# Kernel tuning notes

Measured on AMD Instinct MI355X. Metric: run time of the kernel, lower is better.

## Reference

```python
import jax, jax.numpy as jnp
import numpy as np

N_NODES = 100000
N_EDGES = 3200000
D_FEAT = 128
N1 = 128
N2 = 64
NUM_CLASSES = 10
NUM_GRAPHS = 256


def gcn_conv(x, edge_index, W, b, num_nodes):
    """PyG GCNConv: y = D^-1/2 (A+I) D^-1/2 (x W) + b, self-loops added."""
    src, dst = edge_index[0], edge_index[1]
    # degree including self-loop (edge weight 1)
    deg = jax.ops.segment_sum(jnp.ones_like(dst, dtype=x.dtype), dst,
                              num_segments=num_nodes) + 1.0
    dis = jnp.where(deg > 0, deg ** -0.5, 0.0)  # deg_inv_sqrt, [N]
    h = x @ W                                    # transform first, [N, out]
    norm = dis[src] * dis[dst]                   # [E]
    msg = h[src] * norm[:, None]                 # gather + scale, [E, out]
    agg = jax.ops.segment_sum(msg, dst, num_segments=num_nodes)
    agg = agg + h * (dis * dis)[:, None]         # self-loop contribution
    return agg + b


def global_mean_pool(x, batch, num_graphs):
    sums = jax.ops.segment_sum(x, batch, num_segments=num_graphs)
    cnt = jax.ops.segment_sum(jnp.ones((x.shape[0],), dtype=x.dtype), batch,
                              num_segments=num_graphs)
    return sums / jnp.maximum(cnt, 1.0)[:, None]


def setup_inputs() -> dict:
    key = jax.random.key(0)
    ks = jax.random.split(key, 8)
    x = jax.random.normal(ks[0], (N_NODES, D_FEAT), dtype=jnp.float32)
    edge_index = jax.random.randint(ks[1], (2, N_EDGES), 0, N_NODES, dtype=jnp.int64)
    batch = jnp.sort(jax.random.randint(ks[2], (N_NODES,), 0, NUM_GRAPHS, dtype=jnp.int64))
    W1 = jax.random.normal(ks[3], (D_FEAT, N1), dtype=jnp.float32) / np.sqrt(D_FEAT)
    b1 = jnp.zeros((N1,), dtype=jnp.float32)
    W2 = jax.random.normal(ks[4], (N1, N2), dtype=jnp.float32) / np.sqrt(N1)
    b2 = jnp.zeros((N2,), dtype=jnp.float32)
    Wfc = jax.random.normal(ks[5], (N2, NUM_CLASSES), dtype=jnp.float32) / np.sqrt(N2)
    bfc = jnp.zeros((NUM_CLASSES,), dtype=jnp.float32)
    return {"x": x, "edge_index": edge_index, "batch": batch,
            "W1": W1, "b1": b1, "W2": W2, "b2": b2,
            "Wfc": Wfc, "bfc": bfc, "num_graphs": NUM_GRAPHS}


def reference(x, edge_index, batch, W1, b1, W2, b2, Wfc, bfc, num_graphs):
    n = x.shape[0]
    h = gcn_conv(x, edge_index, W1, b1, n)
    h = jax.nn.relu(h)
    h = gcn_conv(h, edge_index, W2, b2, n)
    g = global_mean_pool(h, batch, num_graphs)   # [num_graphs, N2]
    # dropout is identity at inference
    return g @ Wfc + bfc                          # [num_graphs, num_classes]
```

## Files before the change

kernel.cpp:

```cpp
#include <hip/hip_runtime.h>
#include <math.h>

typedef unsigned int  u32;
typedef unsigned short u16;

#define TILE1 8192
#define BKW   256
#define CAP   9216

typedef __attribute__((ext_vector_type(8))) short bf16x8;
typedef __attribute__((ext_vector_type(4))) float f32x4;
typedef __attribute__((ext_vector_type(2))) float f32x2;
union frag_u { bf16x8 v; u32 u[4]; uint4 q; };

__device__ inline u32 bf16_rne(float f) {
    u32 u = __float_as_uint(f);
    return (u + 0x7FFFu + ((u >> 16) & 1u)) >> 16;
}
__device__ inline float bf_lo(u32 u) { return __uint_as_float(u << 16); }
__device__ inline float bf_hi(u32 u) { return __uint_as_float(u & 0xFFFF0000u); }

__device__ inline f32x2 up2(u32 u) {
    f32x2 t;
    t.x = __uint_as_float(u << 16);
    t.y = __uint_as_float(u & 0xFFFF0000u);
    return t;
}
__device__ inline void add8p(f32x2* a, uint4 q) {
    a[0] += up2(q.x); a[1] += up2(q.y); a[2] += up2(q.z); a[3] += up2(q.w);
}

__device__ inline u32 relu_pk(u32 v) {
    u32 s = v & 0x80008000u;
    u32 m = (s >> 15) * 0xFFFFu;
    return v & ~m;
}


__global__ __launch_bounds__(512) void k_part1(const int* __restrict__ ei,
                                               int* __restrict__ bucketCur,
                                               u32* __restrict__ tmp,
                                               int E, int N, int NBK) {
    __shared__ int hist[1024];
    __shared__ int base[512];
    const int tid = threadIdx.x;
    if (tid < NBK) { hist[tid] = 0; hist[512 + tid] = 0; }
    __syncthreads();

    const int rep = (tid & 1) << 9;
    const int t0 = blockIdx.x * TILE1;
    const int4* ei4s = (const int4*)ei;
    const int4* ei4d = (const int4*)(ei + E);
    const int q0 = t0 >> 2;
    const int QE = E >> 2;

    int sv[16], dv[16], key[16];
#pragma unroll
    for (int j = 0; j < 4; ++j) {
        int qi = q0 + j * 512 + tid;
        int4 s4 = make_int4(0, 0, 0, 0), d4 = make_int4(-1, -1, -1, -1);
        if (qi < QE) { s4 = ei4s[qi]; d4 = ei4d[qi]; }
        sv[4 * j + 0] = s4.x; dv[4 * j + 0] = d4.x;
        sv[4 * j + 1] = s4.y; dv[4 * j + 1] = d4.y;
        sv[4 * j + 2] = s4.z; dv[4 * j + 2] = d4.z;
        sv[4 * j + 3] = s4.w; dv[4 * j + 3] = d4.w;
    }
#pragma unroll
    for (int j = 0; j < 16; ++j) {
        key[j] = -1;
        if ((unsigned)dv[j] < (unsigned)N && (unsigned)sv[j] < (unsigned)N) {
            key[j] = dv[j] >> 8;
            atomicAdd(&hist[key[j] + rep], 1);
        }
    }
    __syncthreads();
    if (tid < NBK) {
        int tot = hist[tid] + hist[512 + tid];
        base[tid] = atomicAdd(&bucketCur[tid], tot);
        hist[tid] = 0;
    }
    __syncthreads();
#pragma unroll
    for (int j = 0; j < 16; ++j) {
        if (key[j] >= 0) {
            int slot = atomicAdd(&hist[key[j]], 1);
            int off = base[key[j]] + slot;
            if (off < CAP)
                tmp[(size_t)key[j] * CAP + off] =
                    ((u32)(dv[j] & 255) << 17) | (u32)sv[j];
        }
    }
}

__global__ __launch_bounds__(512) void k_part2(const int* __restrict__ bucketCnt,
                                               const u32* __restrict__ tmp,
                                               int* __restrict__ csr,
                                               int* __restrict__ rowptr,
                                               float* __restrict__ dis,
                                               int N, int NBK) {
    __shared__ int hist[256];
    __shared__ int ts[512];
    __shared__ int sStart;
    const int b = blockIdx.x;
    const int t = threadIdx.x;

    int myCnt = (t < NBK) ? bucketCnt[t] : 0;
    ts[t] = myCnt;
    __syncthreads();
    for (int off = 1; off < 512; off <<= 1) {
        int u = (t >= off) ? ts[t - off] : 0;
// ... 19 lines not shown
    __syncthreads();
    for (int off = 1; off < 512; off <<= 1) {
        int u = (t >= off) ? ts[t - off] : 0;
        __syncthreads();
        ts[t] += u;
        __syncthreads();
    }
    if (t < 256) hist[t] = ts[t] - h;
    __syncthreads();

    if (t < 256) {
        int gn = (b << 8) + t;
        if (gn < N) {
            int e0 = hist[t];
            int e1 = (t < 255) ? hist[t + 1] : cnt;
            rowptr[gn] = start + e0;
            dis[gn] = rsqrtf((float)(e1 - e0) + 1.0f);
        }
    }
    __syncthreads();

    for (int i = t; i < cnt; i += 512) {
        u32 v = src[i];
        int p = atomicAdd(&hist[v >> 17], 1);
        csr[start + p] = (int)(v & 0x1FFFFu);
    }
}


__global__ __launch_bounds__(256) void k_convW(
    const float* __restrict__ W1, const float* __restrict__ W2,
    u32* __restrict__ W1h, u32* __restrict__ W1l,
    u32* __restrict__ W2h, u32* __restrict__ W2l,
    int* __restrict__ bucketCur, int NBK)
{
    int idx = blockIdx.x * 256 + threadIdx.x;
    if (idx < NBK) bucketCur[idx] = 0;
    if (idx < 8192) {
        int n = idx >> 6, k = (idx & 63) * 2;
        float w0 = W1[k * 128 + n], w1 = W1[(k + 1) * 128 + n];
        u32 h0 = bf16_rne(w0), h1 = bf16_rne(w1);
        u32 l0 = bf16_rne(w0 - __uint_as_float(h0 << 16));
        u32 l1 = bf16_rne(w1 - __uint_as_float(h1 << 16));
        W1h[idx] = h0 | (h1 << 16);
        W1l[idx] = l0 | (l1 << 16);
    } else if (idx < 12288) {
        int i2 = idx - 8192;
        int n = i2 >> 6, k = (i2 & 63) * 2;
        float w0 = W2[k * 64 + n], w1 = W2[(k + 1) * 64 + n];
        u32 h0 = bf16_rne(w0), h1 = bf16_rne(w1);
        u32 l0 = bf16_rne(w0 - __uint_as_float(h0 << 16));
        u32 l1 = bf16_rne(w1 - __uint_as_float(h1 << 16));
        W2h[i2] = h0 | (h1 << 16);
        W2l[i2] = l0 | (l1 << 16);
    }
}


__global__ __launch_bounds__(256) void k_gemm1m(
    const float* __restrict__ X, const u32* __restrict__ Wh,
    const u32* __restrict__ Wl, const float* __restrict__ dis,
    u32* __restrict__ Hb, int M)
{
    __shared__ uint4 sW[4096];
    const int tid = threadIdx.x;
    const uint4* Wh4 = (const uint4*)Wh;
    const uint4* Wl4 = (const uint4*)Wl;
#pragma unroll
    for (int i = 0; i < 8; ++i) {
        int idx = tid + i * 256;
// ... 49 lines not shown
        for (int kt = 0; kt < 4; ++kt) {
            frag_u Bh, Bl;
            int jb = (kt * 4 + quad) ^ swz;
            Bh.q = sW[l * 16 + jb];
            Bl.q = sW[2048 + l * 16 + jb];
            acc0 = __builtin_amdgcn_mfma_f32_16x16x32_bf16(Al[0][kt].v, Bh.v, acc0, 0, 0, 0);
            acc0 = __builtin_amdgcn_mfma_f32_16x16x32_bf16(Ah[0][kt].v, Bl.v, acc0, 0, 0, 0);
            acc0 = __builtin_amdgcn_mfma_f32_16x16x32_bf16(Ah[0][kt].v, Bh.v, acc0, 0, 0, 0);
            acc1 = __builtin_amdgcn_mfma_f32_16x16x32_bf16(Al[1][kt].v, Bh.v, acc1, 0, 0, 0);
            acc1 = __builtin_amdgcn_mfma_f32_16x16x32_bf16(Ah[1][kt].v, Bl.v, acc1, 0, 0, 0);
            acc1 = __builtin_amdgcn_mfma_f32_16x16x32_bf16(Ah[1][kt].v, Bh.v, acc1, 0, 0, 0);
        }
#pragma unroll
        for (int r = 0; r < 4; ++r) {
            float vs0 = acc0[r] * dv[0][r];
            float vo0 = __shfl_xor(vs0, 1, 64);
            float vs1 = acc1[r] * dv[1][r];
            float vo1 = __shfl_xor(vs1, 1, 64);
            if ((m16 & 1) == 0) {
                int gR0 = mrow + quad * 4 + r;
                if (gR0 < M)
                    Hb[(size_t)gR0 * 64 + nt * 8 + (m16 >> 1)] =
                        bf16_rne(vs0) | (bf16_rne(vo0) << 16);
                int gR1 = mrow + 16 + quad * 4 + r;
                if (gR1 < M)
                    Hb[(size_t)gR1 * 64 + nt * 8 + (m16 >> 1)] =
                        bf16_rne(vs1) | (bf16_rne(vo1) << 16);
            }
        }
    }
}


__global__ __launch_bounds__(256) void k_gemm2m(
    const u32* __restrict__ Xb, const u32* __restrict__ Wh,
    const u32* __restrict__ Wl, const float* __restrict__ dis,
    u32* __restrict__ Hb, int M)
{
    __shared__ uint4 sW[2176];
    const int tid = threadIdx.x;
    const uint4* Wh4 = (const uint4*)Wh;
    const uint4* Wl4 = (const uint4*)Wl;
#pragma unroll
    for (int i = 0; i < 4; ++i) {
        int idx = tid + i * 256;
        int l = idx >> 4, j = idx & 15;
        sW[l * 17 + j] = Wh4[l * 16 + j];
        sW[1088 + l * 17 + j] = Wl4[l * 16 + j];
    }
    __syncthreads();

    const int w = tid >> 6, lane = tid & 63;
    const int mrow = blockIdx.x * 128 + w * 32;
    const int m16 = lane & 15, quad = lane >> 4;

    const uint4* X4 = (const uint4*)Xb;
    frag_u A[2][4];
#pragma unroll
    for (int t = 0; t < 2; ++t) {
        int gm = mrow + t * 16 + m16; if (gm >= M) gm = M - 1;
#pragma unroll
        for (int kt = 0; kt < 4; ++kt) {
            A[t][kt].q = X4[(size_t)gm * 16 + kt * 4 + quad];
#pragma unroll
            for (int j = 0; j < 4; ++j) A[t][kt].u[j] = relu_pk(A[t][kt].u[j]);
        }
    }

    float dv[2][4];
#pragma unroll
    for (int t = 0; t < 2; ++t)
#pragma unroll
        for (int r = 0; r < 4; ++r) {
            int gR = mrow + t * 16 + quad * 4 + r;
            dv[t][r] = (gR < M) ? dis[gR] : 0.f;
        }

#pragma unroll
    for (int nt = 0; nt < 4; ++nt) {
        f32x4 acc0 = {0.f, 0.f, 0.f, 0.f};
        f32x4 acc1 = {0.f, 0.f, 0.f, 0.f};
        int l = nt * 16 + m16;
#pragma unroll
        for (int kt = 0; kt < 4; ++kt) {
            frag_u Bh, Bl;
            Bh.q = sW[l * 17 + kt * 4 + quad];
            Bl.q = sW[1088 + l * 17 + kt * 4 + quad];
            acc0 = __builtin_amdgcn_mfma_f32_16x16x32_bf16(A[0][kt].v, Bl.v, acc0, 0, 0, 0);
            acc0 = __builtin_amdgcn_mfma_f32_16x16x32_bf16(A[0][kt].v, Bh.v, acc0, 0, 0, 0);
            acc1 = __builtin_amdgcn_mfma_f32_16x16x32_bf16(A[1][kt].v, Bl.v, acc1, 0, 0, 0);
            acc1 = __builtin_amdgcn_mfma_f32_16x16x32_bf16(A[1][kt].v, Bh.v, acc1, 0, 0, 0);
        }
#pragma unroll
        for (int r = 0; r < 4; ++r) {
            float vs0 = acc0[r] * dv[0][r];
            float vo0 = __shfl_xor(vs0, 1, 64);
            float vs1 = acc1[r] * dv[1][r];
            float vo1 = __shfl_xor(vs1, 1, 64);
            if ((m16 & 1) == 0) {
                int gR0 = mrow + quad * 4 + r;
                if (gR0 < M)
                    Hb[(size_t)gR0 * 32 + nt * 8 + (m16 >> 1)] =
                        bf16_rne(vs0) | (bf16_rne(vo0) << 16);
                int gR1 = mrow + 16 + quad * 4 + r;
                if (gR1 < M)
                    Hb[(size_t)gR1 * 32 + nt * 8 + (m16 >> 1)] =
                        bf16_rne(vs1) | (bf16_rne(vo1) << 16);
            }
        }
    }
}


template <int SH, int POFF>
__global__ __launch_bounds__(256) void k_aggh(
    const int* __restrict__ rowptr, const int* __restrict__ csr,
    const float* __restrict__ dis, const u32* __restrict__ Hb,
    const float* __restrict__ bias, u32* __restrict__ AGGb, int N)
{
    int gid = blockIdx.x * 256 + threadIdx.x;
    int n = gid >> 3;
    int li = threadIdx.x & 7;
    if (n >= N) return;
    int e = rowptr[n];
    int s1 = rowptr[n + 1];
    const float dn = dis[n];
    const char* hb = (const char*)Hb;
    const u32 off = (u32)(POFF + li * 16);

    f32x2 acc[4];
#pragma unroll
    for (int j = 0; j < 4; ++j) acc[j] = 0.f;

    for (; e + 8 <= s1; e += 8) {
        u32 b0 = (u32)csr[e + 0] << SH;
        u32 b1 = (u32)csr[e + 1] << SH;
        u32 b2 = (u32)csr[e + 2] << SH;
        u32 b3 = (u32)csr[e + 3] << SH;
        u32 b4 = (u32)csr[e + 4] << SH;
        u32 b5 = (u32)csr[e + 5] << SH;
        u32 b6 = (u32)csr[e + 6] << SH;
        u32 b7 = (u32)csr[e + 7] << SH;
        uint4 q0 = *(const uint4*)(hb + b0 + off);
        uint4 q1 = *(const uint4*)(hb + b1 + off);
        uint4 q2 = *(const uint4*)(hb + b2 + off);
        uint4 q3 = *(const uint4*)(hb + b3 + off);
        uint4 q4 = *(const uint4*)(hb + b4 + off);
        uint4 q5 = *(const uint4*)(hb + b5 + off);
        uint4 q6 = *(const uint4*)(hb + b6 + off);
        uint4 q7 = *(const uint4*)(hb + b7 + off);
        add8p(acc, q0); add8p(acc, q1); add8p(acc, q2); add8p(acc, q3);
        add8p(acc, q4); add8p(acc, q5); add8p(acc, q6); add8p(acc, q7);
    }
    for (; e + 2 <= s1; e += 2) {
        u32 b0 = (u32)csr[e + 0] << SH;
        u32 b1 = (u32)csr[e + 1] << SH;
        uint4 q0 = *(const uint4*)(hb + b0 + off);
        uint4 q1 = *(const uint4*)(hb + b1 + off);
        add8p(acc, q0); add8p(acc, q1);
    }
    if (e < s1) {
        u32 b0 = (u32)csr[e] << SH;
        uint4 q0 = *(const uint4*)(hb + b0 + off);
        add8p(acc, q0);
    }
    {
        uint4 q = *(const uint4*)(hb + ((u32)n << SH) + off);
        add8p(acc, q);
    }

    float4 b0 = ((const float4*)bias)[POFF / 8 + li * 2 + 0];
    float4 b1 = ((const float4*)bias)[POFF / 8 + li * 2 + 1];
    uint4 p;
    p.x = bf16_rne(fmaf(dn, acc[0].x, b0.x)) | (bf16_rne(fmaf(dn, acc[0].y, b0.y)) << 16);
    p.y = bf16_rne(fmaf(dn, acc[1].x, b0.z)) | (bf16_rne(fmaf(dn, acc[1].y, b0.w)) << 16);
    p.z = bf16_rne(fmaf(dn, acc[2].x, b1.x)) | (bf16_rne(fmaf(dn, acc[2].y, b1.y)) << 16);
    p.w = bf16_rne(fmaf(dn, acc[3].x, b1.z)) | (bf16_rne(fmaf(dn, acc[3].y, b1.w)) << 16);
    ((uint4*)AGGb)[(size_t)n * (1 << (SH - 4)) + POFF / 16 + li] = p;
}


__device__ inline int lower_bound(const int* __restrict__ b, int n, int v) {
    int lo = 0, hi = n;
    while (lo < hi) { int m = (lo + hi) >> 1; if (b[m] < v) lo = m + 1; else hi = m; }
    return lo;
}

__global__ __launch_bounds__(256) void k_poolfc(
    const int* __restrict__ batch, const u32* __restrict__ AGGb2,
    const float* __restrict__ Wfc, const float* __restrict__ bfc,
    float* __restrict__ out, int n)
{
    int g = blockIdx.x;
    int start = lower_bound(batch, n, g);
    int end   = lower_bound(batch, n, g + 1);
    int tid = threadIdx.x;
    int f = tid & 63, stripe = tid >> 6;
    int ui = f >> 1, hi = f & 1;
    float acc = 0.f;
    for (int i = start + stripe; i < end; i += 4) {
        u32 v = AGGb2[(size_t)i * 32 + ui];
        acc += hi ? bf_hi(v) : bf_lo(v);
    }
    __shared__ float red[256];
    __shared__ float mean[64];
    red[tid] = acc;
    __syncthreads();
    if (tid < 64) {
        float s = red[tid] + red[tid + 64] + red[tid + 128] + red[tid + 192];
        float c = (float)(end - start);
        mean[tid] = s / fmaxf(c, 1.0f);
    }
    __syncthreads();
    if (tid < 10) {
        float o = bfc[tid];
        for (int k = 0; k < 64; ++k)
            o = fmaf(mean[k], Wfc[k * 10 + tid], o);
        out[g * 10 + tid] = o;
    }
}


extern "C" void kernel_launch(void* const* d_in, const int* in_sizes, int n_in,
                              void* d_out, int out_size, void* d_ws, size_t ws_size,
                              hipStream_t stream)
{
    const float* x    = (const float*)d_in[0];
    const int*   ei   = (const int*)d_in[1];
    const int*   batch= (const int*)d_in[2];
    const float* W1   = (const float*)d_in[3];
    const float* b1   = (const float*)d_in[4];
    const float* W2   = (const float*)d_in[5];
    const float* b2   = (const float*)d_in[6];
    const float* Wfc  = (const float*)d_in[7];
    const float* bfc  = (const float*)d_in[8];
    float* out = (float*)d_out;

    const int N  = in_sizes[0] / 128;
    const int E  = in_sizes[1] / 2;
    const int ng = out_size / 10;

    const int NBK = (N + BKW - 1) / BKW;

    int*   rowptr    = (int*)d_ws;
    int*   bucketCur = rowptr + 102400;
    float* dis       = (float*)(bucketCur + 512);
    int*   csr       = (int*)(dis + 102400);
    u32*   tmp       = (u32*)(csr + E);
    u32*   Hb1       = tmp;
    u32*   agg2b     = tmp;
    u32*   agg1b     = (u32*)((int*)tmp + (size_t)N * 64);
    u16*   Hb2       = (u16*)((int*)agg1b + (size_t)N * 128);
    u32*   W1h       = (u32*)((int*)Hb2 + (size_t)N * 32);
    u32*   W1l       = W1h + 8192;
    u32*   W2h       = W1l + 8192;
    u32*   W2l       = W2h + 4096;

    k_convW<<<48, 256, 0, stream>>>(W1, W2, W1h, W1l, W2h, W2l, bucketCur, NBK);
    k_part1<<<(E + TILE1 - 1) / TILE1, 512, 0, stream>>>(ei, bucketCur, tmp, E, N, NBK);
    k_part2<<<NBK, 512, 0, stream>>>(bucketCur, tmp, csr, rowptr, dis, N, NBK);

    k_gemm1m<<<(N + 127) / 128, 256, 0, stream>>>(x, W1h, W1l, dis, Hb1, N);
    k_aggh<8, 0><<<(N * 8 + 255) / 256, 256, 0, stream>>>(rowptr, csr, dis, Hb1, b1, agg1b, N);
    k_aggh<8, 128><<<(N * 8 + 255) / 256, 256, 0, stream>>>(rowptr, csr, dis, Hb1, b1, agg1b, N);

    k_gemm2m<<<(N + 127) / 128, 256, 0, stream>>>(agg1b, W2h, W2l, dis, (u32*)Hb2, N);
    k_aggh<7, 0><<<(N * 8 + 255) / 256, 256, 0, stream>>>(rowptr, csr, dis, (const u32*)Hb2, b2, agg2b, N);

    k_poolfc<<<ng, 256, 0, stream>>>(batch, agg2b, Wfc, bfc, out, N);
}
```

Baseline: 384.3 us.

## Fuse aggregation, second GEMM, aggregation and pooling into one cooperative kernel

Replaces the five launches after the first GEMM (two layer-1 aggregation halves, GEMM2, layer-2 aggregation, pool+FC) with a single persistent cooperative kernel. The phases are separated by grid-wide syncs and use grid-stride loops. This removes launch gaps and tail effects between kernels, at the cost of grid-sync overhead and occupancy fixed by the cooperative grid size. The layer-1 aggregation now processes both 128-byte halves in one pass. It also widens the part1 shared histogram replication from 2 to 4 copies to cut atomic contention, and moves agg2b to its own buffer.

```diff
diff --git a/kernel.cpp b/kernel.cpp
--- a/kernel.cpp
+++ b/kernel.cpp
@@ -1,5 +1,8 @@
 #include <hip/hip_runtime.h>
+#include <hip/hip_cooperative_groups.h>
 #include <math.h>
+
+namespace cg = cooperative_groups;
 
 typedef unsigned int  u32;
 typedef unsigned short u16;
@@ -41,13 +44,16 @@
                                                int* __restrict__ bucketCur,
                                                u32* __restrict__ tmp,
                                                int E, int N, int NBK) {
-    __shared__ int hist[1024];
+    __shared__ int hist[2048];
     __shared__ int base[512];
     const int tid = threadIdx.x;
-    if (tid < NBK) { hist[tid] = 0; hist[512 + tid] = 0; }
-    __syncthreads();
-
-    const int rep = (tid & 1) << 9;
+    if (tid < NBK) {
+        hist[tid] = 0; hist[512 + tid] = 0;
+        hist[1024 + tid] = 0; hist[1536 + tid] = 0;
+    }
+    __syncthreads();
+
+    const int rep = (tid & 3) << 9;
     const int t0 = blockIdx.x * TILE1;
     const int4* ei4s = (const int4*)ei;
     const int4* ei4d = (const int4*)(ei + E);
@@ -75,7 +81,7 @@
     }
     __syncthreads();
     if (tid < NBK) {
-        int tot = hist[tid] + hist[512 + tid];
+        int tot = hist[tid] + hist[512 + tid] + hist[1024 + tid] + hist[1536 + tid];
         base[tid] = atomicAdd(&bucketCur[tid], tot);
         hist[tid] = 0;
     }
@@ -280,81 +286,252 @@
 }
 
 
-__global__ __launch_bounds__(256) void k_gemm2m(
-    const u32* __restrict__ Xb, const u32* __restrict__ Wh,
-    const u32* __restrict__ Wl, const float* __restrict__ dis,
-    u32* __restrict__ Hb, int M)
+__device__ inline int lower_bound(const int* __restrict__ b, int n, int v) {
+    int lo = 0, hi = n;
+    while (lo < hi) { int m = (lo + hi) >> 1; if (b[m] < v) lo = m + 1; else hi = m; }
+    return lo;
+}
+
+
+__global__ __launch_bounds__(256, 4) void k_coop(
+    const int* rowptr, const int* csr, const float* dis,
+    const u32* Hb1, const float* b1, u32* agg1b,
+    const u32* W2h, const u32* W2l,
+    u32* Hb2, const float* b2, u32* agg2b,
+    const int* batch, const float* Wfc, const float* bfc,
+    float* out, int N, int ng)
 {
     __shared__ uint4 sW[2176];
+    cg::grid_group gg = cg::this_grid();
     const int tid = threadIdx.x;
-    const uint4* Wh4 = (const uint4*)Wh;
-    const uint4* Wl4 = (const uint4*)Wl;
-#pragma unroll
-    for (int i = 0; i < 4; ++i) {
-        int idx = tid + i * 256;
-        int l = idx >> 4, j = idx & 15;
-        sW[l * 17 + j] = Wh4[l * 16 + j];
-        sW[1088 + l * 17 + j] = Wl4[l * 16 + j];
-    }
-    __syncthreads();
-
-    const int w = tid >> 6, lane = tid & 63;
-    const int mrow = blockIdx.x * 128 + w * 32;
-    const int m16 = lane & 15, quad = lane >> 4;
-
-    const uint4* X4 = (const uint4*)Xb;
-    frag_u A[2][4];
-#pragma unroll
-    for (int t = 0; t < 2; ++t) {
-        int gm = mrow + t * 16 + m16; if (gm >= M) gm = M - 1;
-#pragma unroll
-        for (int kt = 0; kt < 4; ++kt) {
-            A[t][kt].q = X4[(size_t)gm * 16 + kt * 4 + quad];
-#pragma unroll
-            for (int j = 0; j < 4; ++j) A[t][kt].u[j] = relu_pk(A[t][kt].u[j]);
-        }
-    }
-
-    float dv[2][4];
-#pragma unroll
-    for (int t = 0; t < 2; ++t)
-#pragma unroll
-        for (int r = 0; r < 4; ++r) {
-            int gR = mrow + t * 16 + quad * 4 + r;
-            dv[t][r] = (gR < M) ? dis[gR] : 0.f;
-        }
-
-#pragma unroll
-    for (int nt = 0; nt < 4; ++nt) {
-        f32x4 acc0 = {0.f, 0.f, 0.f, 0.f};
-        f32x4 acc1 = {0.f, 0.f, 0.f, 0.f};
-        int l = nt * 16 + m16;
-#pragma unroll
-        for (int kt = 0; kt < 4; ++kt) {
-            frag_u Bh, Bl;
-            Bh.q = sW[l * 17 + kt * 4 + quad];
-            Bl.q = sW[1088 + l * 17 + kt * 4 + quad];
-            acc0 = __builtin_amdgcn_mfma_f32_16x16x32_bf16(A[0][kt].v, Bl.v, acc0, 0, 0, 0);
-            acc0 = __builtin_amdgcn_mfma_f32_16x16x32_bf16(A[0][kt].v, Bh.v, acc0, 0, 0, 0);
-            acc1 = __builtin_amdgcn_mfma_f32_16x16x32_bf16(A[1][kt].v, Bl.v, acc1, 0, 0, 0);
-            acc1 = __builtin_amdgcn_mfma_f32_16x16x32_bf16(A[1][kt].v, Bh.v, acc1, 0, 0, 0);
-        }
-#pragma unroll
-        for (int r = 0; r < 4; ++r) {
-            float vs0 = acc0[r] * dv[0][r];
-            float vo0 = __shfl_xor(vs0, 1, 64);
-            float vs1 = acc1[r] * dv[1][r];
-            float vo1 = __shfl_xor(vs1, 1, 64);
-            if ((m16 & 1) == 0) {
-                int gR0 = mrow + quad * 4 + r;
-                if (gR0 < M)
-                    Hb[(size_t)gR0 * 32 + nt * 8 + (m16 >> 1)] =
-                        bf16_rne(vs0) | (bf16_rne(vo0) << 16);
-                int gR1 = mrow + 16 + quad * 4 + r;
-                if (gR1 < M)
-                    Hb[(size_t)gR1 * 32 + nt * 8 + (m16 >> 1)] =
-                        bf16_rne(vs1) | (bf16_rne(vo1) << 16);
-            }
+    const int gsz = gridDim.x * 256;
+
+    {
+        const uint4* Wh4 = (const uint4*)W2h;
+        const uint4* Wl4 = (const uint4*)W2l;
+#pragma unroll
+        for (int i = 0; i < 4; ++i) {
+            int idx = tid + i * 256;
+            int l = idx >> 4, j = idx & 15;
+            sW[l * 17 + j] = Wh4[l * 16 + j];
+            sW[1088 + l * 17 + j] = Wl4[l * 16 + j];
+        }
+        __syncthreads();
+    }
+
+    {
+        const char* hb = (const char*)Hb1;
+        const int li = tid & 7;
+        const int total = N * 16;
+        for (int idx = blockIdx.x * 256 + tid; idx < total; idx += gsz) {
+            int n = idx >> 4;
+            u32 off = (u32)((((idx >> 3) & 1) << 7) + (li << 4));
+            int e = rowptr[n];
+            int s1 = rowptr[n + 1];
+            float dn = dis[n];
+            f32x2 acc[4];
+#pragma unroll
+            for (int j = 0; j < 4; ++j) acc[j] = 0.f;
+
+            for (; e + 8 <= s1; e += 8) {
+                u32 a0 = (u32)csr[e + 0] << 8; u32 a1 = (u32)csr[e + 1] << 8;
+                u32 a2 = (u32)csr[e + 2] << 8; u32 a3 = (u32)csr[e + 3] << 8;
+                u32 a4 = (u32)csr[e + 4] << 8; u32 a5 = (u32)csr[e + 5] << 8;
+                u32 a6 = (u32)csr[e + 6] << 8; u32 a7 = (u32)csr[e + 7] << 8;
+                uint4 q0 = *(const uint4*)(hb + a0 + off);
+                uint4 q1 = *(const uint4*)(hb + a1 + off);
+                uint4 q2 = *(const uint4*)(hb + a2 + off);
+                uint4 q3 = *(const uint4*)(hb + a3 + off);
+                uint4 q4 = *(const uint4*)(hb + a4 + off);
+                uint4 q5 = *(const uint4*)(hb + a5 + off);
+                uint4 q6 = *(const uint4*)(hb + a6 + off);
+                uint4 q7 = *(const uint4*)(hb + a7 + off);
+                add8p(acc, q0); add8p(acc, q1); add8p(acc, q2); add8p(acc, q3);
+                add8p(acc, q4); add8p(acc, q5); add8p(acc, q6); add8p(acc, q7);
+            }
+            for (; e + 2 <= s1; e += 2) {
+                u32 a0 = (u32)csr[e + 0] << 8; u32 a1 = (u32)csr[e + 1] << 8;
+                uint4 q0 = *(const uint4*)(hb + a0 + off);
+                uint4 q1 = *(const uint4*)(hb + a1 + off);
+                add8p(acc, q0); add8p(acc, q1);
+            }
+            if (e < s1) {
+                u32 a0 = (u32)csr[e] << 8;
+                uint4 q0 = *(const uint4*)(hb + a0 + off);
+                add8p(acc, q0);
+            }
+            {
+                uint4 q = *(const uint4*)(hb + ((u32)n << 8) + off);
+                add8p(acc, q);
+            }
+
+            float4 bb0 = ((const float4*)b1)[off >> 3];
+            float4 bb1 = ((const float4*)b1)[(off >> 3) + 1];
+            uint4 p;
+            p.x = bf16_rne(fmaf(dn, acc[0].x, bb0.x)) | (bf16_rne(fmaf(dn, acc[0].y, bb0.y)) << 16);
+            p.y = bf16_rne(fmaf(dn, acc[1].x, bb0.z)) | (bf16_rne(fmaf(dn, acc[1].y, bb0.w)) << 16);
+            p.z = bf16_rne(fmaf(dn, acc[2].x, bb1.x)) | (bf16_rne(fmaf(dn, acc[2].y, bb1.y)) << 16);
+            p.w = bf16_rne(fmaf(dn, acc[3].x, bb1.z)) | (bf16_rne(fmaf(dn, acc[3].y, bb1.w)) << 16);
+            ((uint4*)agg1b)[(size_t)n * 16 + (off >> 4)] = p;
+        }
+    }
+    __threadfence();
+    gg.sync();
+
+    {
+        const int w = tid >> 6, lane = tid & 63;
+        const int m16 = lane & 15, quad = lane >> 4;
+        const uint4* X4 = (const uint4*)agg1b;
+        const int ntile = (N + 127) >> 7;
+        for (int mt = blockIdx.x; mt < ntile; mt += gridDim.x) {
+            const int mrow = mt * 128 + w * 32;
+
+            frag_u A[2][4];
+#pragma unroll
+            for (int t = 0; t < 2; ++t) {
+                int gm = mrow + t * 16 + m16; if (gm >= N) gm = N - 1;
+#pragma unroll
+                for (int kt = 0; kt < 4; ++kt) {
+                    A[t][kt].q = X4[(size_t)gm * 16 + kt * 4 + quad];
+#pragma unroll
+                    for (int j = 0; j < 4; ++j) A[t][kt].u[j] = relu_pk(A[t][kt].u[j]);
+                }
+            }
+
+            float dv[2][4];
+#pragma unroll
+            for (int t = 0; t < 2; ++t)
+#pragma unroll
+                for (int r = 0; r < 4; ++r) {
+                    int gR = mrow + t * 16 + quad * 4 + r;
+                    dv[t][r] = (gR < N) ? dis[gR] : 0.f;
+                }
+
+#pragma unroll
+            for (int nt = 0; nt < 4; ++nt) {
+                f32x4 acc0 = {0.f, 0.f, 0.f, 0.f};
+                f32x4 acc1 = {0.f, 0.f, 0.f, 0.f};
+                int l = nt * 16 + m16;
+#pragma unroll
+                for (int kt = 0; kt < 4; ++kt) {
+                    frag_u Bh, Bl;
+                    Bh.q = sW[l * 17 + kt * 4 + quad];
+                    Bl.q = sW[1088 + l * 17 + kt * 4 + quad];
+                    acc0 = __builtin_amdgcn_mfma_f32_16x16x32_bf16(A[0][kt].v, Bl.v, acc0, 0, 0, 0);
+                    acc0 = __builtin_amdgcn_mfma_f32_16x16x32_bf16(A[0][kt].v, Bh.v, acc0, 0, 0, 0);
+                    acc1 = __builtin_amdgcn_mfma_f32_16x16x32_bf16(A[1][kt].v, Bl.v, acc1, 0, 0, 0);
+                    acc1 = __builtin_amdgcn_mfma_f32_16x16x32_bf16(A[1][kt].v, Bh.v, acc1, 0, 0, 0);
+                }
+#pragma unroll
+                for (int r = 0; r < 4; ++r) {
+                    float vs0 = acc0[r] * dv[0][r];
+                    float vo0 = __shfl_xor(vs0, 1, 64);
+                    float vs1 = acc1[r] * dv[1][r];
+                    float vo1 = __shfl_xor(vs1, 1, 64);
+                    if ((m16 & 1) == 0) {
+                        int gR0 = mrow + quad * 4 + r;
+                        if (gR0 < N)
+                            Hb2[(size_t)gR0 * 32 + nt * 8 + (m16 >> 1)] =
+                                bf16_rne(vs0) | (bf16_rne(vo0) << 16);
+                        int gR1 = mrow + 16 + quad * 4 + r;
+                        if (gR1 < N)
+                            Hb2[(size_t)gR1 * 32 + nt * 8 + (m16 >> 1)] =
+                                bf16_rne(vs1) | (bf16_rne(vo1) << 16);
+                    }
+                }
+            }
+        }
+    }
+    __threadfence();
+    gg.sync();
+
+    {
+        const char* hb = (const char*)Hb2;
+        const int li = tid & 7;
+        const u32 off = (u32)(li << 4);
+        const int total = N * 8;
+        for (int idx = blockIdx.x * 256 + tid; idx < total; idx += gsz) {
+            int n = idx >> 3;
+            int e = rowptr[n];
+            int s1 = rowptr[n + 1];
+            float dn = dis[n];
+            f32x2 acc[4];
+#pragma unroll
+            for (int j = 0; j < 4; ++j) acc[j] = 0.f;
+
+            for (; e + 8 <= s1; e += 8) {
+                u32 a0 = (u32)csr[e + 0] << 7; u32 a1 = (u32)csr[e + 1] << 7;
+                u32 a2 = (u32)csr[e + 2] << 7; u32 a3 = (u32)csr[e + 3] << 7;
+                u32 a4 = (u32)csr[e + 4] << 7; u32 a5 = (u32)csr[e + 5] << 7;
+                u32 a6 = (u32)csr[e + 6] << 7; u32 a7 = (u32)csr[e + 7] << 7;
+                uint4 q0 = *(const uint4*)(hb + a0 + off);
+                uint4 q1 = *(const uint4*)(hb + a1 + off);
+                uint4 q2 = *(const uint4*)(hb + a2 + off);
+                uint4 q3 = *(const uint4*)(hb + a3 + off);
+                uint4 q4 = *(const uint4*)(hb + a4 + off);
+                uint4 q5 = *(const uint4*)(hb + a5 + off);
+                uint4 q6 = *(const uint4*)(hb + a6 + off);
+                uint4 q7 = *(const uint4*)(hb + a7 + off);
+                add8p(acc, q0); add8p(acc, q1); add8p(acc, q2); add8p(acc, q3);
+                add8p(acc, q4); add8p(acc, q5); add8p(acc, q6); add8p(acc, q7);
+            }
+            for (; e + 2 <= s1; e += 2) {
+                u32 a0 = (u32)csr[e + 0] << 7; u32 a1 = (u32)csr[e + 1] << 7;
+                uint4 q0 = *(const uint4*)(hb + a0 + off);
+                uint4 q1 = *(const uint4*)(hb + a1 + off);
+                add8p(acc, q0); add8p(acc, q1);
+            }
+            if (e < s1) {
+                u32 a0 = (u32)csr[e] << 7;
+                uint4 q0 = *(const uint4*)(hb + a0 + off);
+                add8p(acc, q0);
+            }
+            {
+                uint4 q = *(const uint4*)(hb + ((u32)n << 7) + off);
+                add8p(acc, q);
+            }
+
+            float4 bb0 = ((const float4*)b2)[off >> 3];
+            float4 bb1 = ((const float4*)b2)[(off >> 3) + 1];
+            uint4 p;
+            p.x = bf16_rne(fmaf(dn, acc[0].x, bb0.x)) | (bf16_rne(fmaf(dn, acc[0].y, bb0.y)) << 16);
+            p.y = bf16_rne(fmaf(dn, acc[1].x, bb0.z)) | (bf16_rne(fmaf(dn, acc[1].y, bb0.w)) << 16);
+            p.z = bf16_rne(fmaf(dn, acc[2].x, bb1.x)) | (bf16_rne(fmaf(dn, acc[2].y, bb1.y)) << 16);
+            p.w = bf16_rne(fmaf(dn, acc[3].x, bb1.z)) | (bf16_rne(fmaf(dn, acc[3].y, bb1.w)) << 16);
+            ((uint4*)agg2b)[(size_t)n * 8 + (off >> 4)] = p;
+        }
+    }
+    __threadfence();
+    gg.sync();
+
+    {
+        float* red  = (float*)sW;
+        float* mean = ((float*)sW) + 256;
+        const int f = tid & 63, stripe = tid >> 6;
+        const int ui = f >> 1, hi = f & 1;
+        for (int g = blockIdx.x; g < ng; g += gridDim.x) {
+            int start = lower_bound(batch, N, g);
+            int end   = lower_bound(batch, N, g + 1);
+            float acc = 0.f;
+            for (int i = start + stripe; i < end; i += 4) {
+                u32 v = agg2b[(size_t)i * 32 + ui];
+                acc += hi ? bf_hi(v) : bf_lo(v);
+            }
+            red[tid] = acc;
+            __syncthreads();
+            if (tid < 64) {
+                float s = red[tid] + red[tid + 64] + red[tid + 128] + red[tid + 192];
+                float c = (float)(end - start);
+                mean[tid] = s / fmaxf(c, 1.0f);
+            }
+            __syncthreads();
+            if (tid < 10) {
+                float o = bfc[tid];
+                for (int k = 0; k < 64; ++k)
+                    o = fmaf(mean[k], Wfc[k * 10 + tid], o);
+                out[g * 10 + tid] = o;
+            }
+            __syncthreads();
         }
     }
 }
@@ -381,35 +558,30 @@
     for (int j = 0; j < 4; ++j) acc[j] = 0.f;
 
     for (; e + 8 <= s1; e += 8) {
-        u32 b0 = (u32)csr[e + 0] << SH;
-        u32 b1 = (u32)csr[e + 1] << SH;
-        u32 b2 = (u32)csr[e + 2] << SH;
-        u32 b3 = (u32)csr[e + 3] << SH;
-        u32 b4 = (u32)csr[e + 4] << SH;
-        u32 b5 = (u32)csr[e + 5] << SH;
-        u32 b6 = (u32)csr[e + 6] << SH;
-        u32 b7 = (u32)csr[e + 7] << SH;
-        uint4 q0 = *(const uint4*)(hb + b0 + off);
-        uint4 q1 = *(const uint4*)(hb + b1 + off);
-        uint4 q2 = *(const uint4*)(hb + b2 + off);
-        uint4 q3 = *(const uint4*)(hb + b3 + off);
-        uint4 q4 = *(const uint4*)(hb + b4 + off);
-        uint4 q5 = *(const uint4*)(hb + b5 + off);
-        uint4 q6 = *(const uint4*)(hb + b6 + off);
-        uint4 q7 = *(const uint4*)(hb + b7 + off);
+        u32 a0 = (u32)csr[e + 0] << SH; u32 a1 = (u32)csr[e + 1] << SH;
+        u32 a2 = (u32)csr[e + 2] << SH; u32 a3 = (u32)csr[e + 3] << SH;
+        u32 a4 = (u32)csr[e + 4] << SH; u32 a5 = (u32)csr[e + 5] << SH;
+        u32 a6 = (u32)csr[e + 6] << SH; u32 a7 = (u32)csr[e + 7] << SH;
+        uint4 q0 = *(const uint4*)(hb + a0 + off);
+        uint4 q1 = *(const uint4*)(hb + a1 + off);
+        uint4 q2 = *(const uint4*)(hb + a2 + off);
+        uint4 q3 = *(const uint4*)(hb + a3 + off);
+        uint4 q4 = *(const uint4*)(hb + a4 + off);
+        uint4 q5 = *(const uint4*)(hb + a5 + off);
+        uint4 q6 = *(const uint4*)(hb + a6 + off);
+        uint4 q7 = *(const uint4*)(hb + a7 + off);
         add8p(acc, q0); add8p(acc, q1); add8p(acc, q2); add8p(acc, q3);
         add8p(acc, q4); add8p(acc, q5); add8p(acc, q6); add8p(acc, q7);
     }
     for (; e + 2 <= s1; e += 2) {
-        u32 b0 = (u32)csr[e + 0] << SH;
-        u32 b1 = (u32)csr[e + 1] << SH;
-        uint4 q0 = *(const uint4*)(hb + b0 + off);
-        uint4 q1 = *(const uint4*)(hb + b1 + off);
+        u32 a0 = (u32)csr[e + 0] << SH; u32 a1 = (u32)csr[e + 1] << SH;
+        uint4 q0 = *(const uint4*)(hb + a0 + off);
+        uint4 q1 = *(const uint4*)(hb + a1 + off);
         add8p(acc, q0); add8p(acc, q1);
     }
     if (e < s1) {
-        u32 b0 = (u32)csr[e] << SH;
-        uint4 q0 = *(const uint4*)(hb + b0 + off);
+        u32 a0 = (u32)csr[e] << SH;
+        uint4 q0 = *(const uint4*)(hb + a0 + off);
         add8p(acc, q0);
     }
     {
@@ -417,21 +589,93 @@
         add8p(acc, q);
     }
 
-    float4 b0 = ((const float4*)bias)[POFF / 8 + li * 2 + 0];
-    float4 b1 = ((const float4*)bias)[POFF / 8 + li * 2 + 1];
+    float4 bb0 = ((const float4*)bias)[POFF / 8 + li * 2 + 0];
+    float4 bb1 = ((const float4*)bias)[POFF / 8 + li * 2 + 1];
     uint4 p;
-    p.x = bf16_rne(fmaf(dn, acc[0].x, b0.x)) | (bf16_rne(fmaf(dn, acc[0].y, b0.y)) << 16);
-    p.y = bf16_rne(fmaf(dn, acc[1].x, b0.z)) | (bf16_rne(fmaf(dn, acc[1].y, b0.w)) << 16);
-    p.z = bf16_rne(fmaf(dn, acc[2].x, b1.x)) | (bf16_rne(fmaf(dn, acc[2].y, b1.y)) << 16);
-    p.w = bf16_rne(fmaf(dn, acc[3].x, b1.z)) | (bf16_rne(fmaf(dn, acc[3].y, b1.w)) << 16);
+    p.x = bf16_rne(fmaf(dn, acc[0].x, bb0.x)) | (bf16_rne(fmaf(dn, acc[0].y, bb0.y)) << 16);
+    p.y = bf16_rne(fmaf(dn, acc[1].x, bb0.z)) | (bf16_rne(fmaf(dn, acc[1].y, bb0.w)) << 16);
+    p.z = bf16_rne(fmaf(dn, acc[2].x, bb1.x)) | (bf16_rne(fmaf(dn, acc[2].y, bb1.y)) << 16);
+    p.w = bf16_rne(fmaf(dn, acc[3].x, bb1.z)) | (bf16_rne(fmaf(dn, acc[3].y, bb1.w)) << 16);
     ((uint4*)AGGb)[(size_t)n * (1 << (SH - 4)) + POFF / 16 + li] = p;
 }
 
-
-__device__ inline int lower_bound(const int* __restrict__ b, int n, int v) {
-    int lo = 0, hi = n;
-    while (lo < hi) { int m = (lo + hi) >> 1; if (b[m] < v) lo = m + 1; else hi = m; }
-    return lo;
+__global__ __launch_bounds__(256) void k_gemm2m(
+    const u32* __restrict__ Xb, const u32* __restrict__ Wh,
+    const u32* __restrict__ Wl, const float* __restrict__ dis,
+    u32* __restrict__ Hb, int M)
+{
+    __shared__ uint4 sW[2176];
+    const int tid = threadIdx.x;
+    const uint4* Wh4 = (const uint4*)Wh;
+    const uint4* Wl4 = (const uint4*)Wl;
+#pragma unroll
+    for (int i = 0; i < 4; ++i) {
+        int idx = tid + i * 256;
+        int l = idx >> 4, j = idx & 15;
+        sW[l * 17 + j] = Wh4[l * 16 + j];
+        sW[1088 + l * 17 + j] = Wl4[l * 16 + j];
+    }
+    __syncthreads();
+
+    const int w = tid >> 6, lane = tid & 63;
+    const int mrow = blockIdx.x * 128 + w * 32;
+    const int m16 = lane & 15, quad = lane >> 4;
+
+    const uint4* X4 = (const uint4*)Xb;
+    frag_u A[2][4];
+#pragma unroll
+    for (int t = 0; t < 2; ++t) {
+        int gm = mrow + t * 16 + m16; if (gm >= M) gm = M - 1;
+#pragma unroll
+        for (int kt = 0; kt < 4; ++kt) {
+            A[t][kt].q = X4[(size_t)gm * 16 + kt * 4 + quad];
+#pragma unroll
+            for (int j = 0; j < 4; ++j) A[t][kt].u[j] = relu_pk(A[t][kt].u[j]);
+        }
+    }
+
+    float dv[2][4];
+#pragma unroll
+    for (int t = 0; t < 2; ++t)
+#pragma unroll
+        for (int r = 0; r < 4; ++r) {
+            int gR = mrow + t * 16 + quad * 4 + r;
+            dv[t][r] = (gR < M) ? dis[gR] : 0.f;
+        }
+
+#pragma unroll
+    for (int nt = 0; nt < 4; ++nt) {
+        f32x4 acc0 = {0.f, 0.f, 0.f, 0.f};
+        f32x4 acc1 = {0.f, 0.f, 0.f, 0.f};
+        int l = nt * 16 + m16;
+#pragma unroll
+        for (int kt = 0; kt < 4; ++kt) {
+            frag_u Bh, Bl;
+            Bh.q = sW[l * 17 + kt * 4 + quad];
+            Bl.q = sW[1088 + l * 17 + kt * 4 + quad];
+            acc0 = __builtin_amdgcn_mfma_f32_16x16x32_bf16(A[0][kt].v, Bl.v, acc0, 0, 0, 0);
+            acc0 = __builtin_amdgcn_mfma_f32_16x16x32_bf16(A[0][kt].v, Bh.v, acc0, 0, 0, 0);
+            acc1 = __builtin_amdgcn_mfma_f32_16x16x32_bf16(A[1][kt].v, Bl.v, acc1, 0, 0, 0);
+            acc1 = __builtin_amdgcn_mfma_f32_16x16x32_bf16(A[1][kt].v, Bh.v, acc1, 0, 0, 0);
+        }
+#pragma unroll
+        for (int r = 0; r < 4; ++r) {
+            float vs0 = acc0[r] * dv[0][r];
+            float vo0 = __shfl_xor(vs0, 1, 64);
+            float vs1 = acc1[r] * dv[1][r];
+            float vo1 = __shfl_xor(vs1, 1, 64);
+            if ((m16 & 1) == 0) {
+                int gR0 = mrow + quad * 4 + r;
+                if (gR0 < M)
+                    Hb[(size_t)gR0 * 32 + nt * 8 + (m16 >> 1)] =
+                        bf16_rne(vs0) | (bf16_rne(vo0) << 16);
+                int gR1 = mrow + 16 + quad * 4 + r;
+                if (gR1 < M)
+                    Hb[(size_t)gR1 * 32 + nt * 8 + (m16 >> 1)] =
+                        bf16_rne(vs1) | (bf16_rne(vo1) << 16);
+            }
+        }
+    }
 }
 
 __global__ __launch_bounds__(256) void k_poolfc(
@@ -496,24 +740,51 @@
     int*   csr       = (int*)(dis + 102400);
     u32*   tmp       = (u32*)(csr + E);
     u32*   Hb1       = tmp;
-    u32*   agg2b     = tmp;
     u32*   agg1b     = (u32*)((int*)tmp + (size_t)N * 64);
     u16*   Hb2       = (u16*)((int*)agg1b + (size_t)N * 128);
     u32*   W1h       = (u32*)((int*)Hb2 + (size_t)N * 32);
     u32*   W1l       = W1h + 8192;
     u32*   W2h       = W1l + 8192;
     u32*   W2l       = W2h + 4096;
+    u32*   agg2b     = W2l + 4096;
 
     k_convW<<<48, 256, 0, stream>>>(W1, W2, W1h, W1l, W2h, W2l, bucketCur, NBK);
     k_part1<<<(E + TILE1 - 1) / TILE1, 512, 0, stream>>>(ei, bucketCur, tmp, E, N, NBK);
     k_part2<<<NBK, 512, 0, stream>>>(bucketCur, tmp, csr, rowptr, dis, N, NBK);
-
     k_gemm1m<<<(N + 127) / 128, 256, 0, stream>>>(x, W1h, W1l, dis, Hb1, N);
-    k_aggh<8, 0><<<(N * 8 + 255) / 256, 256, 0, stream>>>(rowptr, csr, dis, Hb1, b1, agg1b, N);
-    k_aggh<8, 128><<<(N * 8 + 255) / 256, 256, 0, stream>>>(rowptr, csr, dis, Hb1, b1, agg1b, N);
-
-    k_gemm2m<<<(N + 127) / 128, 256, 0, stream>>>(agg1b, W2h, W2l, dis, (u32*)Hb2, N);
-    k_aggh<7, 0><<<(N * 8 + 255) / 256, 256, 0, stream>>>(rowptr, csr, dis, (const u32*)Hb2, b2, agg2b, N);
-
-    k_poolfc<<<ng, 256, 0, stream>>>(batch, agg2b, Wfc, bfc, out, N);
-}
+
+    static int coopBlocks = -1;
+    if (coopBlocks < 0) {
+        int nb = 0, ncu = 0, dev = 0;
+        hipGetDevice(&dev);
+        hipDeviceGetAttribute(&ncu, hipDeviceAttributeMultiprocessorCount, dev);
+        hipOccupancyMaxActiveBlocksPerMultiprocessor(&nb, (const void*)k_coop, 256, 0);
+        if (nb < 1) nb = 1;
+        if (ncu < 1) ncu = 256;
+        coopBlocks = nb * ncu;
+        if (coopBlocks > 2048) coopBlocks = 2048;
+    }
+
+    const u32* Hb2c = (const u32*)Hb2;
+    void* args[] = {
+        (void*)&rowptr, (void*)&csr, (void*)&dis,
+        (void*)&Hb1, (void*)&b1, (void*)&agg1b,
+        (void*)&W2h, (void*)&W2l,
+        (void*)&Hb2, (void*)&b2, (void*)&agg2b,
+        (void*)&batch, (void*)&Wfc, (void*)&bfc,
+        (void*)&out, (void*)&N, (void*)&ng
+    };
+    void* hb2p = (void*)Hb2;
+    args[8] = (void*)&hb2p;
+
+    hipError_t cerr = hipLaunchCooperativeKernel(
+        (const void*)k_coop, dim3(coopBlocks), dim3(256), args, 0, stream);
+
+    if (cerr != hipSuccess) {
+        k_aggh<8, 0><<<(N * 8 + 255) / 256, 256, 0, stream>>>(rowptr, csr, dis, Hb1, b1, agg1b, N);
+        k_aggh<8, 128><<<(N * 8 + 255) / 256, 256, 0, stream>>>(rowptr, csr, dis, Hb1, b1, agg1b, N);
+        k_gemm2m<<<(N + 127) / 128, 256, 0, stream>>>(agg1b, W2h, W2l, dis, (u32*)Hb2, N);
+        k_aggh<7, 0><<<(N * 8 + 255) / 256, 256, 0, stream>>>(rowptr, csr, dis, Hb2c, b2, agg2b, N);
+        k_poolfc<<<ng, 256, 0, stream>>>(batch, agg2b, Wfc, bfc, out, N);
+    }
+}
```

Result: slower. 811.3 us (+111.1%).

## Fuse layer-2 aggregation with mean pooling and FC via atomics and last-block ticket

Applied to the files above, without the earlier changes.

Replaces the layer-2 aggregation kernel and the separate pooling/FC kernel with one kernel. It reduces each node's aggregated features directly into per-graph accumulators using wave-level shuffles plus atomics. The last block to finish, found by a ticket counter, computes the means, adds the bias and applies the FC layer. This removes the bf16 store and reload of the layer-2 output and one launch, at the cost of global float atomics and a nondeterministic summation order. The partition histogram is also widened from 2 to 4 replicas to reduce LDS atomic contention.

```diff
diff --git a/kernel.cpp b/kernel.cpp
--- a/kernel.cpp
+++ b/kernel.cpp
@@ -41,13 +41,16 @@
                                                int* __restrict__ bucketCur,
                                                u32* __restrict__ tmp,
                                                int E, int N, int NBK) {
-    __shared__ int hist[1024];
+    __shared__ int hist[2048];
     __shared__ int base[512];
     const int tid = threadIdx.x;
-    if (tid < NBK) { hist[tid] = 0; hist[512 + tid] = 0; }
-    __syncthreads();
-
-    const int rep = (tid & 1) << 9;
+    if (tid < NBK) {
+        hist[tid] = 0; hist[512 + tid] = 0;
+        hist[1024 + tid] = 0; hist[1536 + tid] = 0;
+    }
+    __syncthreads();
+
+    const int rep = (tid & 3) << 9;
     const int t0 = blockIdx.x * TILE1;
     const int4* ei4s = (const int4*)ei;
     const int4* ei4d = (const int4*)(ei + E);
@@ -75,7 +78,7 @@
     }
     __syncthreads();
     if (tid < NBK) {
-        int tot = hist[tid] + hist[512 + tid];
+        int tot = hist[tid] + hist[512 + tid] + hist[1024 + tid] + hist[1536 + tid];
         base[tid] = atomicAdd(&bucketCur[tid], tot);
         hist[tid] = 0;
     }
@@ -161,10 +164,13 @@
     const float* __restrict__ W1, const float* __restrict__ W2,
     u32* __restrict__ W1h, u32* __restrict__ W1l,
     u32* __restrict__ W2h, u32* __restrict__ W2l,
-    int* __restrict__ bucketCur, int NBK)
+    int* __restrict__ bucketCur, float* __restrict__ graphAcc,
+    int* __restrict__ done, int NBK)
 {
     int idx = blockIdx.x * 256 + threadIdx.x;
     if (idx < NBK) bucketCur[idx] = 0;
+    if (idx < 16384) graphAcc[idx] = 0.f;
+    if (idx == 16384) *done = 0;
     if (idx < 8192) {
         int n = idx >> 6, k = (idx & 63) * 2;
         float w0 = W1[k * 128 + n], w1 = W1[(k + 1) * 128 + n];
@@ -381,35 +387,30 @@
     for (int j = 0; j < 4; ++j) acc[j] = 0.f;
 
     for (; e + 8 <= s1; e += 8) {
-        u32 b0 = (u32)csr[e + 0] << SH;
-        u32 b1 = (u32)csr[e + 1] << SH;
-        u32 b2 = (u32)csr[e + 2] << SH;
-        u32 b3 = (u32)csr[e + 3] << SH;
-        u32 b4 = (u32)csr[e + 4] << SH;
-        u32 b5 = (u32)csr[e + 5] << SH;
-        u32 b6 = (u32)csr[e + 6] << SH;
-        u32 b7 = (u32)csr[e + 7] << SH;
-        uint4 q0 = *(const uint4*)(hb + b0 + off);
-        uint4 q1 = *(const uint4*)(hb + b1 + off);
-        uint4 q2 = *(const uint4*)(hb + b2 + off);
-        uint4 q3 = *(const uint4*)(hb + b3 + off);
-        uint4 q4 = *(const uint4*)(hb + b4 + off);
-        uint4 q5 = *(const uint4*)(hb + b5 + off);
-        uint4 q6 = *(const uint4*)(hb + b6 + off);
-        uint4 q7 = *(const uint4*)(hb + b7 + off);
+        u32 a0 = (u32)csr[e + 0] << SH; u32 a1 = (u32)csr[e + 1] << SH;
+        u32 a2 = (u32)csr[e + 2] << SH; u32 a3 = (u32)csr[e + 3] << SH;
+        u32 a4 = (u32)csr[e + 4] << SH; u32 a5 = (u32)csr[e + 5] << SH;
+        u32 a6 = (u32)csr[e + 6] << SH; u32 a7 = (u32)csr[e + 7] << SH;
+        uint4 q0 = *(const uint4*)(hb + a0 + off);
+        uint4 q1 = *(const uint4*)(hb + a1 + off);
+        uint4 q2 = *(const uint4*)(hb + a2 + off);
+        uint4 q3 = *(const uint4*)(hb + a3 + off);
+        uint4 q4 = *(const uint4*)(hb + a4 + off);
+        uint4 q5 = *(const uint4*)(hb + a5 + off);
+        uint4 q6 = *(const uint4*)(hb + a6 + off);
+        uint4 q7 = *(const uint4*)(hb + a7 + off);
         add8p(acc, q0); add8p(acc, q1); add8p(acc, q2); add8p(acc, q3);
         add8p(acc, q4); add8p(acc, q5); add8p(acc, q6); add8p(acc, q7);
     }
     for (; e + 2 <= s1; e += 2) {
-        u32 b0 = (u32)csr[e + 0] << SH;
-        u32 b1 = (u32)csr[e + 1] << SH;
-        uint4 q0 = *(const uint4*)(hb + b0 + off);
-        uint4 q1 = *(const uint4*)(hb + b1 + off);
+        u32 a0 = (u32)csr[e + 0] << SH; u32 a1 = (u32)csr[e + 1] << SH;
+        uint4 q0 = *(const uint4*)(hb + a0 + off);
+        uint4 q1 = *(const uint4*)(hb + a1 + off);
         add8p(acc, q0); add8p(acc, q1);
     }
     if (e < s1) {
-        u32 b0 = (u32)csr[e] << SH;
-        uint4 q0 = *(const uint4*)(hb + b0 + off);
+        u32 a0 = (u32)csr[e] << SH;
+        uint4 q0 = *(const uint4*)(hb + a0 + off);
         add8p(acc, q0);
     }
     {
@@ -417,13 +418,13 @@
         add8p(acc, q);
     }
 
-    float4 b0 = ((const float4*)bias)[POFF / 8 + li * 2 + 0];
-    float4 b1 = ((const float4*)bias)[POFF / 8 + li * 2 + 1];
+    float4 bb0 = ((const float4*)bias)[POFF / 8 + li * 2 + 0];
+    float4 bb1 = ((const float4*)bias)[POFF / 8 + li * 2 + 1];
     uint4 p;
-    p.x = bf16_rne(fmaf(dn, acc[0].x, b0.x)) | (bf16_rne(fmaf(dn, acc[0].y, b0.y)) << 16);
-    p.y = bf16_rne(fmaf(dn, acc[1].x, b0.z)) | (bf16_rne(fmaf(dn, acc[1].y, b0.w)) << 16);
-    p.z = bf16_rne(fmaf(dn, acc[2].x, b1.x)) | (bf16_rne(fmaf(dn, acc[2].y, b1.y)) << 16);
-    p.w = bf16_rne(fmaf(dn, acc[3].x, b1.z)) | (bf16_rne(fmaf(dn, acc[3].y, b1.w)) << 16);
+    p.x = bf16_rne(fmaf(dn, acc[0].x, bb0.x)) | (bf16_rne(fmaf(dn, acc[0].y, bb0.y)) << 16);
+    p.y = bf16_rne(fmaf(dn, acc[1].x, bb0.z)) | (bf16_rne(fmaf(dn, acc[1].y, bb0.w)) << 16);
+    p.z = bf16_rne(fmaf(dn, acc[2].x, bb1.x)) | (bf16_rne(fmaf(dn, acc[2].y, bb1.y)) << 16);
+    p.w = bf16_rne(fmaf(dn, acc[3].x, bb1.z)) | (bf16_rne(fmaf(dn, acc[3].y, bb1.w)) << 16);
     ((uint4*)AGGb)[(size_t)n * (1 << (SH - 4)) + POFF / 16 + li] = p;
 }
 
@@ -434,37 +435,119 @@
     return lo;
 }
 
-__global__ __launch_bounds__(256) void k_poolfc(
-    const int* __restrict__ batch, const u32* __restrict__ AGGb2,
+
+__global__ __launch_bounds__(256) void k_agg2pool(
+    const int* __restrict__ rowptr, const int* __restrict__ csr,
+    const float* __restrict__ dis, const u32* __restrict__ Hb,
+    const int* __restrict__ batch, const float* __restrict__ b2,
     const float* __restrict__ Wfc, const float* __restrict__ bfc,
-    float* __restrict__ out, int n)
+    float* __restrict__ graphAcc, int* __restrict__ done,
+    float* __restrict__ out, int N, int ng, int nblocks)
 {
-    int g = blockIdx.x;
-    int start = lower_bound(batch, n, g);
-    int end   = lower_bound(batch, n, g + 1);
-    int tid = threadIdx.x;
-    int f = tid & 63, stripe = tid >> 6;
-    int ui = f >> 1, hi = f & 1;
-    float acc = 0.f;
-    for (int i = start + stripe; i < end; i += 4) {
-        u32 v = AGGb2[(size_t)i * 32 + ui];
-        acc += hi ? bf_hi(v) : bf_lo(v);
-    }
-    __shared__ float red[256];
-    __shared__ float mean[64];
-    red[tid] = acc;
-    __syncthreads();
-    if (tid < 64) {
-        float s = red[tid] + red[tid + 64] + red[tid + 128] + red[tid + 192];
-        float c = (float)(end - start);
-        mean[tid] = s / fmaxf(c, 1.0f);
-    }
-    __syncthreads();
-    if (tid < 10) {
-        float o = bfc[tid];
-        for (int k = 0; k < 64; ++k)
-            o = fmaf(mean[k], Wfc[k * 10 + tid], o);
-        out[g * 10 + tid] = o;
+    int gid = blockIdx.x * 256 + threadIdx.x;
+    int n = gid >> 3;
+    const int li = threadIdx.x & 7;
+    const bool valid = (n < N);
+    if (!valid) n = N - 1;
+    const float dn = valid ? dis[n] : 0.f;
+    int e = rowptr[n];
+    int s1 = rowptr[n + 1];
+    if (!valid) { e = 0; s1 = 0; }
+    const char* hb = (const char*)Hb;
+    const u32 off = (u32)(li << 4);
+
+    f32x2 acc[4];
+#pragma unroll
+    for (int j = 0; j < 4; ++j) acc[j] = 0.f;
+
+    for (; e + 8 <= s1; e += 8) {
+        u32 a0 = (u32)csr[e + 0] << 7; u32 a1 = (u32)csr[e + 1] << 7;
+        u32 a2 = (u32)csr[e + 2] << 7; u32 a3 = (u32)csr[e + 3] << 7;
+        u32 a4 = (u32)csr[e + 4] << 7; u32 a5 = (u32)csr[e + 5] << 7;
+        u32 a6 = (u32)csr[e + 6] << 7; u32 a7 = (u32)csr[e + 7] << 7;
+        uint4 q0 = *(const uint4*)(hb + a0 + off);
+        uint4 q1 = *(const uint4*)(hb + a1 + off);
+        uint4 q2 = *(const uint4*)(hb + a2 + off);
+        uint4 q3 = *(const uint4*)(hb + a3 + off);
+        uint4 q4 = *(const uint4*)(hb + a4 + off);
+        uint4 q5 = *(const uint4*)(hb + a5 + off);
+        uint4 q6 = *(const uint4*)(hb + a6 + off);
+        uint4 q7 = *(const uint4*)(hb + a7 + off);
+        add8p(acc, q0); add8p(acc, q1); add8p(acc, q2); add8p(acc, q3);
+        add8p(acc, q4); add8p(acc, q5); add8p(acc, q6); add8p(acc, q7);
+    }
+    for (; e + 2 <= s1; e += 2) {
+        u32 a0 = (u32)csr[e + 0] << 7; u32 a1 = (u32)csr[e + 1] << 7;
+        uint4 q0 = *(const uint4*)(hb + a0 + off);
+        uint4 q1 = *(const uint4*)(hb + a1 + off);
+        add8p(acc, q0); add8p(acc, q1);
+    }
+    if (e < s1) {
+        u32 a0 = (u32)csr[e] << 7;
+        uint4 q0 = *(const uint4*)(hb + a0 + off);
+        add8p(acc, q0);
+    }
+    if (valid) {
+        uint4 q = *(const uint4*)(hb + ((u32)n << 7) + off);
+        add8p(acc, q);
+    }
+
+    float v[8];
+#pragma unroll
+    for (int j = 0; j < 4; ++j) {
+        v[2 * j + 0] = dn * acc[j].x;
+        v[2 * j + 1] = dn * acc[j].y;
+    }
+
+    int g = batch[n];
+    int g0 = __shfl(g, 0, 64);
+    if (__all(g == g0)) {
+#pragma unroll
+        for (int j = 0; j < 8; ++j) {
+            v[j] += __shfl_xor(v[j], 8, 64);
+            v[j] += __shfl_xor(v[j], 16, 64);
+            v[j] += __shfl_xor(v[j], 32, 64);
+        }
+        if ((threadIdx.x & 63) < 8) {
+            float* dst = graphAcc + g0 * 64 + li * 8;
+#pragma unroll
+            for (int j = 0; j < 8; ++j) atomicAdd(&dst[j], v[j]);
+        }
+    } else if (valid) {
+        float* dst = graphAcc + g * 64 + li * 8;
+#pragma unroll
+        for (int j = 0; j < 8; ++j) atomicAdd(&dst[j], v[j]);
+    }
+
+    __threadfence();
+    __syncthreads();
+    __shared__ int sticket;
+    if (threadIdx.x == 0) sticket = atomicAdd(done, 1);
+    __syncthreads();
+    if (sticket == nblocks - 1) {
+        __shared__ float sW[640];
+        __shared__ float sb[10];
+        const int t = threadIdx.x;
+        for (int i = t; i < 640; i += 256) sW[i] = Wfc[i];
+        if (t < 10) sb[t] = bfc[t];
+        __syncthreads();
+        if (t < ng) {
+            int start = lower_bound(batch, N, t);
+            int end   = lower_bound(batch, N, t + 1);
+            int cnt = end - start;
+            float inv = 1.f / fmaxf((float)cnt, 1.f);
+            float o[10];
+#pragma unroll
+            for (int c = 0; c < 10; ++c) o[c] = sb[c];
+            for (int k = 0; k < 64; ++k) {
+                float s = atomicAdd(&graphAcc[t * 64 + k], 0.f);
+                float m = s * inv + ((cnt > 0) ? b2[k] : 0.f);
+#pragma unroll
+                for (int c = 0; c < 10; ++c) o[c] = fmaf(m, sW[k * 10 + c], o[c]);
+            }
+#pragma unroll
+            for (int c = 0; c < 10; ++c) out[t * 10 + c] = o[c];
+        }
     }
 }
 
@@ -496,15 +579,17 @@
     int*   csr       = (int*)(dis + 102400);
     u32*   tmp       = (u32*)(csr + E);
     u32*   Hb1       = tmp;
-    u32*   agg2b     = tmp;
     u32*   agg1b     = (u32*)((int*)tmp + (size_t)N * 64);
     u16*   Hb2       = (u16*)((int*)agg1b + (size_t)N * 128);
     u32*   W1h       = (u32*)((int*)Hb2 + (size_t)N * 32);
     u32*   W1l       = W1h + 8192;
     u32*   W2h       = W1l + 8192;
     u32*   W2l       = W2h + 4096;
-
-    k_convW<<<48, 256, 0, stream>>>(W1, W2, W1h, W1l, W2h, W2l, bucketCur, NBK);
+    float* graphAcc  = (float*)(W2l + 4096);
+    int*   done      = (int*)(graphAcc + 16384);
+
+    k_convW<<<65, 256, 0, stream>>>(W1, W2, W1h, W1l, W2h, W2l,
+                                    bucketCur, graphAcc, done, NBK);
     k_part1<<<(E + TILE1 - 1) / TILE1, 512, 0, stream>>>(ei, bucketCur, tmp, E, N, NBK);
     k_part2<<<NBK, 512, 0, stream>>>(bucketCur, tmp, csr, rowptr, dis, N, NBK);
 
@@ -513,7 +598,8 @@
     k_aggh<8, 128><<<(N * 8 + 255) / 256, 256, 0, stream>>>(rowptr, csr, dis, Hb1, b1, agg1b, N);
 
     k_gemm2m<<<(N + 127) / 128, 256, 0, stream>>>(agg1b, W2h, W2l, dis, (u32*)Hb2, N);
-    k_aggh<7, 0><<<(N * 8 + 255) / 256, 256, 0, stream>>>(rowptr, csr, dis, (const u32*)Hb2, b2, agg2b, N);
-
-    k_poolfc<<<ng, 256, 0, stream>>>(batch, agg2b, Wfc, bfc, out, N);
-}
+    const int nblocks = (N * 8 + 255) / 256;
+    k_agg2pool<<<nblocks, 256, 0, stream>>>(rowptr, csr, dis, (const u32*)Hb2,
+                                            batch, b2, Wfc, bfc,
+                                            graphAcc, done, out, N, ng, nblocks);
+}
```

New measurement: 725.2 us. 88.7% more time.
